# Kernel optimization log

Measured on AMD Instinct MI355X. Metric: run time of the kernel, lower is better.

Reference implementation:

```python
import jax, jax.numpy as jnp
import numpy as np

V, E, D = 100000, 128, 60  # vocab, embedding_size, d_alpha
B, J, M, P = 512, 101, 50, 5120
EPS = 1e-6


def setup_inputs() -> dict:
    key = jax.random.key(0)
    ks = jax.random.split(key, 12)
    s = 0.5 / E
    inp = {
        'batch_titems': jax.random.randint(ks[0], (B, J), 0, V),
        'batch_citems': jax.random.randint(ks[1], (B, M), 0, V),
        'batch_pad_ids': jax.random.randint(ks[2], (2, P), 0, M),
        't_emb': jax.random.uniform(ks[3], (V, E), jnp.float32, -s, s),
        'c_emb': jax.random.uniform(ks[4], (V, E), jnp.float32, -s, s),
        'Ac_w': jax.random.normal(ks[5], (D, E), jnp.float32) * 0.05,
        'Ac_b': jnp.zeros((D,), jnp.float32),
        'At_w': jax.random.normal(ks[6], (D, E), jnp.float32) * 0.05,
        'At_b': jnp.zeros((D,), jnp.float32),
        'Bc_w': jax.random.normal(ks[7], (E, E), jnp.float32) * 0.05,
        'Bc_b': jnp.zeros((E,), jnp.float32),
        'R_w': jax.random.normal(ks[8], (E, E), jnp.float32) * 0.05,
        'R_b': jnp.zeros((E,), jnp.float32),
    }
    return inp


def reference(batch_titems, batch_citems, batch_pad_ids, t_emb, c_emb,
              Ac_w, Ac_b, At_w, At_b, Bc_w, Bc_b, R_w, R_b):
    v = t_emb[batch_titems]            # [B, J, E] target item vectors
    u = c_emb[batch_citems]            # [B, M, E] context item vectors
    tp = v @ At_w.T + At_b             # [B, J, D]
    cp = u @ Ac_w.T + Ac_b             # [B, M, D]
    # cosine similarity with torch eps clamp on norms
    dot = jnp.einsum('bjd,bmd->bjm', tp, cp)
    nt = jnp.maximum(jnp.linalg.norm(tp, axis=-1), EPS)  # [B, J]
    nc = jnp.maximum(jnp.linalg.norm(cp, axis=-1), EPS)  # [B, M]
    cos = dot / (nt[:, :, None] * nc[:, None, :])        # [B, J, M]
    # pad mask: (batch, context-pos) pairs masked across all J target rows
    mask = jnp.zeros((cos.shape[0], cos.shape[2]), bool)
    mask = mask.at[batch_pad_ids[0], batch_pad_ids[1]].set(True)
    scores = jnp.where(mask[:, None, :], -jnp.inf, cos)
    attn = jax.nn.softmax(scores, axis=-1)               # [B, J, M]
    bu = u @ Bc_w.T + Bc_b                               # [B, M, E]
    alpha = jnp.einsum('bjm,bme->bje', attn, bu)         # [B, J, E]
    return alpha @ R_w.T + R_b                           # [B, J, E]
```

## Files before the change

### kernel.cpp

```cpp
#include <hip/hip_runtime.h>

typedef unsigned short u16;
typedef unsigned int   u32;
typedef short bf8 __attribute__((ext_vector_type(8)));
typedef float f4  __attribute__((ext_vector_type(4)));

#define NB   512
#define NJ   101
#define NM   50
#define NE   128
#define ND   60
#define NP   5120
#define NT   512
#define EPSV 1e-6f

#define U_B    0
#define T_B    17408
#define C_B    33536
#define H_B    42752
#define NT2_B  61184
#define NC2_B  61632
#define BAT_B  61888
#define BAC_B  62144
#define RB2_B  62400
#define MSK_B  62912
#define TIDX_B 63168
#define ARENA  63616

__device__ __forceinline__ u16 f2bh(float f) {
    return (u16)((__float_as_uint(f) + 0x8000u) >> 16);
}
__device__ __forceinline__ u32 pk2(float a, float b) {
    u32 ia = __float_as_uint(a) + 0x8000u;
    u32 ib = __float_as_uint(b) + 0x8000u;
    return (ia >> 16) | (ib & 0xFFFF0000u);
}
__device__ __forceinline__ bf8 gfrag(const float* p) {
    const float4* q = (const float4*)p;
    float4 x = q[0], y = q[1];
    union { u32 u[4]; bf8 v; } r;
    r.u[0] = pk2(x.x, x.y); r.u[1] = pk2(x.z, x.w);
    r.u[2] = pk2(y.x, y.y); r.u[3] = pk2(y.z, y.w);
    return r.v;
}

__global__ __launch_bounds__(128) void w2_kernel(
    const float* __restrict__ Bc_w, const float* __restrict__ Bc_b,
    const float* __restrict__ R_w,  const float* __restrict__ R_b,
    u16* __restrict__ w2t, float* __restrict__ rb2)
{
    const int e = blockIdx.x, k = threadIdx.x;
    const float* Rrow = R_w + e * NE;
    float acc = 0.f;
    #pragma unroll 8
    for (int j = 0; j < NE; j++) acc += Rrow[j] * Bc_w[j * NE + k];
    w2t[e * NE + k] = f2bh(acc);
    float c = Bc_b[k] * Rrow[k];
    for (int o = 32; o; o >>= 1) c += __shfl_xor(c, o, 64);
    __shared__ float part[2];
    if ((k & 63) == 0) part[k >> 6] = c;
    __syncthreads();
    if (k == 0) rb2[e] = part[0] + part[1] + R_b[e];
}

__global__ __launch_bounds__(NT, 4) void aitv_kernel(
    const int* __restrict__ titems, const int* __restrict__ citems,
    const int* __restrict__ pad_ids,
    const float* __restrict__ t_emb, const float* __restrict__ c_emb,
    const float* __restrict__ Ac_w,  const float* __restrict__ Ac_b,
    const float* __restrict__ At_w,  const float* __restrict__ At_b,
    const u16* __restrict__ w2t,     const float* __restrict__ rb2g,
    float* __restrict__ out)
{
    const int b    = blockIdx.x;
    const int t    = threadIdx.x;
    const int wid  = t >> 6;
    const int lane = t & 63;
    const int l15  = lane & 15;
    const int quad = lane >> 4;

    __shared__ __align__(16) char arena[ARENA];
    u16*   us16 = (u16*)(arena + U_B);   u32* us32 = (u32*)(arena + U_B);
    u16*   tp16 = (u16*)(arena + T_B);   u16* at16 = (u16*)(arena + T_B);
    u16*   cp16 = (u16*)(arena + C_B);
    u16*   hT16 = (u16*)(arena + H_B);
    float* nt2  = (float*)(arena + NT2_B);
    float* nc2  = (float*)(arena + NC2_B);
    float* bat  = (float*)(arena + BAT_B);
    float* bac  = (float*)(arena + BAC_B);
    float* rb2  = (float*)(arena + RB2_B);
    int*   msk  = (int*)(arena + MSK_B);
    int*   tidx = (int*)(arena + TIDX_B);

    for (int i = t; i < 64 * 64; i += NT) {
        int row = i >> 6, c2 = i & 63;
        u32 val = 0;
        if (row < NM) {
            int idx = citems[b * NM + row];
            float2 x = *(const float2*)(c_emb + (size_t)idx * NE + 2 * c2);
            val = pk2(x.x, x.y);
        }
        us32[row * 68 + c2] = val;
    }
    if (t < 112) { nt2[t] = 0.f; tidx[t] = titems[b * NJ + ((t < NJ) ? t : NJ - 1)]; }
    if (t >= 128 && t < 192) { int i = t - 128; nc2[i] = 0.f; msk[i] = 0; }
    if (t >= 192 && t < 256) {
        int i = t - 192;
        bat[i] = (i < ND) ? At_b[i] : 0.f;
        bac[i] = (i < ND) ? Ac_b[i] : 0.f;
    }
    if (t >= 256 && t < 384) rb2[t - 256] = rb2g[t - 256];
    __syncthreads();

    for (int i = t; i < NP; i += NT)
        if (pad_ids[i] == b) msk[pad_ids[NP + i]] = 1;

    for (int u = wid; u < 76; u += 8) {
        if (u < 28) {
            int jt = u >> 2, dt = u & 3;
            int d  = dt * 16 + l15;
            const float* vrow = t_emb + (size_t)tidx[jt * 16 + l15] * NE;
            const float* arow = At_w + (size_t)((d < ND) ? d : ND - 1) * NE;
            float bv = bat[d];
            f4 acc = {bv, bv, bv, bv};
            #pragma unroll
            for (int ks = 0; ks < 4; ks++) {
                bf8 a  = gfrag(vrow + ks * 32 + quad * 8);
                bf8 bb = gfrag(arow + ks * 32 + quad * 8);
                acc = __builtin_amdgcn_mfma_f32_16x16x32_bf16(a, bb, acc, 0, 0, 0);
            }
            int j0 = jt * 16 + quad * 4;
            #pragma unroll
            for (int r = 0; r < 4; r++) {
                float v = acc[r];
                tp16[(j0 + r) * 72 + d] = (d < ND) ? f2bh(v) : (u16)0;
                float q = (d < ND) ? v * v : 0.f;
                q += __shfl_xor(q, 1, 64); q += __shfl_xor(q, 2, 64);
                q += __shfl_xor(q, 4, 64); q += __shfl_xor(q, 8, 64);
                if (l15 == 0) atomicAdd(&nt2[j0 + r], q);
            }
        } else if (u < 44) {
            int uu = u - 28, mt = uu >> 2, dt = uu & 3;
            int d = dt * 16 + l15;
            const float* arow = Ac_w + (size_t)((d < ND) ? d : ND - 1) * NE;
            float bv = bac[d];
            f4 acc = {bv, bv, bv, bv};
            #pragma unroll
            for (int ks = 0; ks < 4; ks++) {
                bf8 a  = *(const bf8*)(us16 + (mt * 16 + l15) * 136 + ks * 32 + quad * 8);
                bf8 bb = gfrag(arow + ks * 32 + quad * 8);
                acc = __builtin_amdgcn_mfma_f32_16x16x32_bf16(a, bb, acc, 0, 0, 0);
            }
            int m0 = mt * 16 + quad * 4;
            #pragma unroll
            for (int r = 0; r < 4; r++) {
                float v = acc[r];
                cp16[(m0 + r) * 72 + d] = (d < ND) ? f2bh(v) : (u16)0;
                float q = (d < ND) ? v * v : 0.f;
                q += __shfl_xor(q, 1, 64); q += __shfl_xor(q, 2, 64);
                q += __shfl_xor(q, 4, 64); q += __shfl_xor(q, 8, 64);
                if (l15 == 0) atomicAdd(&nc2[m0 + r], q);
            }
        } else {
            int uu = u - 44, et = uu >> 2, mt = uu & 3;
            const u16* arow = w2t + (size_t)(et * 16 + l15) * NE;
            f4 acc = {0.f, 0.f, 0.f, 0.f};
            #pragma unroll
            for (int ks = 0; ks < 4; ks++) {
                bf8 a  = *(const bf8*)(arow + ks * 32 + quad * 8);
                bf8 bb = *(const bf8*)(us16 + (mt * 16 + l15) * 136 + ks * 32 + quad * 8);
                acc = __builtin_amdgcn_mfma_f32_16x16x32_bf16(a, bb, acc, 0, 0, 0);
            }
            int e0 = et * 16 + quad * 4;
            for (int r = 0; r < 4; r++)
                hT16[(e0 + r) * 72 + mt * 16 + l15] = f2bh(acc[r]);
        }
    }
    __syncthreads();

    if (wid < 7) {
        const int jt = wid;
        f4 S[4];
        #pragma unroll
        for (int mt = 0; mt < 4; mt++) {
            f4 acc = {0.f, 0.f, 0.f, 0.f};
            #pragma unroll
            for (int ks = 0; ks < 2; ks++) {
                bf8 a  = *(const bf8*)(tp16 + (jt * 16 + l15) * 72 + ks * 32 + quad * 8);
                bf8 bb = *(const bf8*)(cp16 + (mt * 16 + l15) * 72 + ks * 32 + quad * 8);
                acc = __builtin_amdgcn_mfma_f32_16x16x32_bf16(a, bb, acc, 0, 0, 0);
            }
            S[mt] = acc;
        }
        bool  valid[4]; float ncS[4];
        #pragma unroll
        for (int mt = 0; mt < 4; mt++) {
            int m = mt * 16 + l15;
            valid[mt] = (m < NM) && (msk[m] == 0);
            ncS[mt]   = valid[mt] ? fmaxf(sqrtf(nc2[m]), EPSV) : 1.f;
        }
        #pragma unroll
        for (int r = 0; r < 4; r++) {
            int j = jt * 16 + quad * 4 + r;
            float ntj = fmaxf(sqrtf(nt2[j]), EPSV);
            float x[4], mx = -INFINITY;
            #pragma unroll
            for (int mt = 0; mt < 4; mt++) {
                x[mt] = valid[mt] ? S[mt][r] / (ntj * ncS[mt]) : -INFINITY;
                mx = fmaxf(mx, x[mt]);
            }
            mx = fmaxf(mx, __shfl_xor(mx, 1, 64)); mx = fmaxf(mx, __shfl_xor(mx, 2, 64));
            mx = fmaxf(mx, __shfl_xor(mx, 4, 64)); mx = fmaxf(mx, __shfl_xor(mx, 8, 64));
            float p[4], sm = 0.f;
            #pragma unroll
            for (int mt = 0; mt < 4; mt++) {
                p[mt] = valid[mt] ? __expf(x[mt] - mx) : 0.f;
                sm += p[mt];
            }
            sm += __shfl_xor(sm, 1, 64); sm += __shfl_xor(sm, 2, 64);
            sm += __shfl_xor(sm, 4, 64); sm += __shfl_xor(sm, 8, 64);
            float inv = (sm > 0.f) ? 1.f / sm : 0.f;
            #pragma unroll
            for (int mt = 0; mt < 4; mt++)
                at16[j * 72 + mt * 16 + l15] = f2bh(p[mt] * inv);
        }
    }
    __syncthreads();

    for (int u = wid; u < 56; u += 8) {
        int jt = u >> 3, et = u & 7;
        float bv = rb2[et * 16 + l15];
        f4 acc = {bv, bv, bv, bv};
        #pragma unroll
        for (int ks = 0; ks < 2; ks++) {
            bf8 a  = *(const bf8*)(at16 + (jt * 16 + l15) * 72 + ks * 32 + quad * 8);
            bf8 bb = *(const bf8*)(hT16 + (et * 16 + l15) * 72 + ks * 32 + quad * 8);
            acc = __builtin_amdgcn_mfma_f32_16x16x32_bf16(a, bb, acc, 0, 0, 0);
        }
        int e = et * 16 + l15, j0 = jt * 16 + quad * 4;
        for (int r = 0; r < 4; r++) {
            int j = j0 + r;
            if (j < NJ) out[((size_t)b * NJ + j) * NE + e] = acc[r];
        }
    }
}

extern "C" void kernel_launch(void* const* d_in, const int* in_sizes, int n_in,
                              void* d_out, int out_size, void* d_ws, size_t ws_size,
                              hipStream_t stream) {
    const int*   titems  = (const int*)d_in[0];
    const int*   citems  = (const int*)d_in[1];
    const int*   pad_ids = (const int*)d_in[2];
    const float* t_emb   = (const float*)d_in[3];
    const float* c_emb   = (const float*)d_in[4];
    const float* Ac_w    = (const float*)d_in[5];
    const float* Ac_b    = (const float*)d_in[6];
    const float* At_w    = (const float*)d_in[7];
    const float* At_b    = (const float*)d_in[8];
    const float* Bc_w    = (const float*)d_in[9];
    const float* Bc_b    = (const float*)d_in[10];
    const float* R_w     = (const float*)d_in[11];
    const float* R_b     = (const float*)d_in[12];
    float* out = (float*)d_out;

    u16*   w2t = (u16*)d_ws;
    float* rb2 = (float*)((char*)d_ws + 32768);

    w2_kernel<<<NE, NE, 0, stream>>>(Bc_w, Bc_b, R_w, R_b, w2t, rb2);
    aitv_kernel<<<NB, NT, 0, stream>>>(titems, citems, pad_ids, t_emb, c_emb,
                                       Ac_w, Ac_b, At_w, At_b, w2t, rb2, out);
}
```

Before: 190.9 us.

## Keep gathered embedding fragments in registers and regroup per-wave projection work

The context embeddings are no longer staged into shared memory. Each wave now gathers a 16-row tile of target or context embeddings straight into register fragments and reuses them across all d-tiles, and for the context rows also across the Bc/R-fused e-tiles. This removes the LDS staging pass and the redundant re-gathering of t_emb rows that happened once per d-tile. Shared memory drops to about 44 KB, which could allow more blocks per CU. The trade-offs are that the work splits into 15 uneven groups across 8 waves, the context rows are gathered twice, and biases are read directly from global memory. The small w2 kernel also gets four independent accumulators.

```diff
diff --git a/kernel.cpp b/kernel.cpp
--- a/kernel.cpp
+++ b/kernel.cpp
@@ -14,18 +14,13 @@
 #define NT   512
 #define EPSV 1e-6f
 
-#define U_B    0
-#define T_B    17408
-#define C_B    33536
-#define H_B    42752
-#define NT2_B  61184
-#define NC2_B  61632
-#define BAT_B  61888
-#define BAC_B  62144
-#define RB2_B  62400
-#define MSK_B  62912
-#define TIDX_B 63168
-#define ARENA  63616
+#define T_B    0
+#define C_B    16128
+#define H_B    25344
+#define NT2_B  43776
+#define NC2_B  44224
+#define MSK_B  44480
+#define ARENA  44736
 
 __device__ __forceinline__ u16 f2bh(float f) {
     return (u16)((__float_as_uint(f) + 0x8000u) >> 16);
@@ -51,10 +46,15 @@
 {
     const int e = blockIdx.x, k = threadIdx.x;
     const float* Rrow = R_w + e * NE;
-    float acc = 0.f;
+    float a0 = 0.f, a1 = 0.f, a2 = 0.f, a3 = 0.f;
     #pragma unroll 8
-    for (int j = 0; j < NE; j++) acc += Rrow[j] * Bc_w[j * NE + k];
-    w2t[e * NE + k] = f2bh(acc);
+    for (int j = 0; j < NE; j += 4) {
+        a0 += Rrow[j]     * Bc_w[j * NE + k];
+        a1 += Rrow[j + 1] * Bc_w[(j + 1) * NE + k];
+        a2 += Rrow[j + 2] * Bc_w[(j + 2) * NE + k];
+        a3 += Rrow[j + 3] * Bc_w[(j + 3) * NE + k];
+    }
+    w2t[e * NE + k] = f2bh((a0 + a1) + (a2 + a3));
     float c = Bc_b[k] * Rrow[k];
     for (int o = 32; o; o >>= 1) c += __shfl_xor(c, o, 64);
     __shared__ float part[2];
@@ -80,100 +80,109 @@
     const int quad = lane >> 4;
 
     __shared__ __align__(16) char arena[ARENA];
-    u16*   us16 = (u16*)(arena + U_B);   u32* us32 = (u32*)(arena + U_B);
     u16*   tp16 = (u16*)(arena + T_B);   u16* at16 = (u16*)(arena + T_B);
     u16*   cp16 = (u16*)(arena + C_B);
     u16*   hT16 = (u16*)(arena + H_B);
     float* nt2  = (float*)(arena + NT2_B);
     float* nc2  = (float*)(arena + NC2_B);
-    float* bat  = (float*)(arena + BAT_B);
-    float* bac  = (float*)(arena + BAC_B);
-    float* rb2  = (float*)(arena + RB2_B);
     int*   msk  = (int*)(arena + MSK_B);
-    int*   tidx = (int*)(arena + TIDX_B);
-
-    for (int i = t; i < 64 * 64; i += NT) {
-        int row = i >> 6, c2 = i & 63;
-        u32 val = 0;
-        if (row < NM) {
-            int idx = citems[b * NM + row];
-            float2 x = *(const float2*)(c_emb + (size_t)idx * NE + 2 * c2);
-            val = pk2(x.x, x.y);
-        }
-        us32[row * 68 + c2] = val;
-    }
-    if (t < 112) { nt2[t] = 0.f; tidx[t] = titems[b * NJ + ((t < NJ) ? t : NJ - 1)]; }
-    if (t >= 128 && t < 192) { int i = t - 128; nc2[i] = 0.f; msk[i] = 0; }
-    if (t >= 192 && t < 256) {
-        int i = t - 192;
-        bat[i] = (i < ND) ? At_b[i] : 0.f;
-        bac[i] = (i < ND) ? Ac_b[i] : 0.f;
-    }
-    if (t >= 256 && t < 384) rb2[t - 256] = rb2g[t - 256];
+
+    if (t < 112) nt2[t] = 0.f;
+    else if (t < 176) nc2[t - 112] = 0.f;
+    else if (t < 240) msk[t - 176] = 0;
     __syncthreads();
 
     for (int i = t; i < NP; i += NT)
         if (pad_ids[i] == b) msk[pad_ids[NP + i]] = 1;
 
-    for (int u = wid; u < 76; u += 8) {
-        if (u < 28) {
-            int jt = u >> 2, dt = u & 3;
-            int d  = dt * 16 + l15;
-            const float* vrow = t_emb + (size_t)tidx[jt * 16 + l15] * NE;
-            const float* arow = At_w + (size_t)((d < ND) ? d : ND - 1) * NE;
-            float bv = bat[d];
-            f4 acc = {bv, bv, bv, bv};
-            #pragma unroll
-            for (int ks = 0; ks < 4; ks++) {
-                bf8 a  = gfrag(vrow + ks * 32 + quad * 8);
-                bf8 bb = gfrag(arow + ks * 32 + quad * 8);
-                acc = __builtin_amdgcn_mfma_f32_16x16x32_bf16(a, bb, acc, 0, 0, 0);
-            }
-            int j0 = jt * 16 + quad * 4;
-            #pragma unroll
-            for (int r = 0; r < 4; r++) {
-                float v = acc[r];
-                tp16[(j0 + r) * 72 + d] = (d < ND) ? f2bh(v) : (u16)0;
-                float q = (d < ND) ? v * v : 0.f;
-                q += __shfl_xor(q, 1, 64); q += __shfl_xor(q, 2, 64);
-                q += __shfl_xor(q, 4, 64); q += __shfl_xor(q, 8, 64);
-                if (l15 == 0) atomicAdd(&nt2[j0 + r], q);
-            }
-        } else if (u < 44) {
-            int uu = u - 28, mt = uu >> 2, dt = uu & 3;
-            int d = dt * 16 + l15;
-            const float* arow = Ac_w + (size_t)((d < ND) ? d : ND - 1) * NE;
-            float bv = bac[d];
-            f4 acc = {bv, bv, bv, bv};
-            #pragma unroll
-            for (int ks = 0; ks < 4; ks++) {
-                bf8 a  = *(const bf8*)(us16 + (mt * 16 + l15) * 136 + ks * 32 + quad * 8);
-                bf8 bb = gfrag(arow + ks * 32 + quad * 8);
-                acc = __builtin_amdgcn_mfma_f32_16x16x32_bf16(a, bb, acc, 0, 0, 0);
-            }
-            int m0 = mt * 16 + quad * 4;
-            #pragma unroll
-            for (int r = 0; r < 4; r++) {
-                float v = acc[r];
-                cp16[(m0 + r) * 72 + d] = (d < ND) ? f2bh(v) : (u16)0;
-                float q = (d < ND) ? v * v : 0.f;
-                q += __shfl_xor(q, 1, 64); q += __shfl_xor(q, 2, 64);
-                q += __shfl_xor(q, 4, 64); q += __shfl_xor(q, 8, 64);
-                if (l15 == 0) atomicAdd(&nc2[m0 + r], q);
+    for (int g = wid; g < 15; g += 8) {
+        if (g < 7) {
+            const int jt = g;
+            const int j  = jt * 16 + l15;
+            const float* vrow = t_emb + (size_t)titems[b * NJ + ((j < NJ) ? j : NJ - 1)] * NE;
+            bf8 A[4];
+            #pragma unroll
+            for (int ks = 0; ks < 4; ks++) A[ks] = gfrag(vrow + ks * 32 + quad * 8);
+            #pragma unroll
+            for (int dt = 0; dt < 4; dt++) {
+                const int d = dt * 16 + l15;
+                const float* arow = At_w + (size_t)((d < ND) ? d : 0) * NE;
+                float bv = (d < ND) ? At_b[d] : 0.f;
+                f4 acc = {bv, bv, bv, bv};
+                #pragma unroll
+                for (int ks = 0; ks < 4; ks++)
+                    acc = __builtin_amdgcn_mfma_f32_16x16x32_bf16(
+                        A[ks], gfrag(arow + ks * 32 + quad * 8), acc, 0, 0, 0);
+                const int j0 = jt * 16 + quad * 4;
+                #pragma unroll
+                for (int r = 0; r < 4; r++) {
+                    float v = acc[r];
+                    tp16[(j0 + r) * 72 + d] = (d < ND) ? f2bh(v) : (u16)0;
+                    float q = (d < ND) ? v * v : 0.f;
+                    q += __shfl_xor(q, 1, 64); q += __shfl_xor(q, 2, 64);
+                    q += __shfl_xor(q, 4, 64); q += __shfl_xor(q, 8, 64);
+                    if (l15 == 0) atomicAdd(&nt2[j0 + r], q);
+                }
+            }
+        } else if (g < 11) {
+            const int mt = g - 7;
+            const int m  = mt * 16 + l15;
+            const float* urow = c_emb + (size_t)citems[b * NM + ((m < NM) ? m : 0)] * NE;
+            bf8 U[4];
+            #pragma unroll
+            for (int ks = 0; ks < 4; ks++) U[ks] = gfrag(urow + ks * 32 + quad * 8);
+            #pragma unroll
+            for (int dt = 0; dt < 4; dt++) {
+                const int d = dt * 16 + l15;
+                const float* arow = Ac_w + (size_t)((d < ND) ? d : 0) * NE;
+                float bv = (d < ND) ? Ac_b[d] : 0.f;
+                f4 acc = {bv, bv, bv, bv};
+                #pragma unroll
+                for (int ks = 0; ks < 4; ks++)
+                    acc = __builtin_amdgcn_mfma_f32_16x16x32_bf16(
+                        U[ks], gfrag(arow + ks * 32 + quad * 8), acc, 0, 0, 0);
+                const int m0 = mt * 16 + quad * 4;
+                #pragma unroll
+                for (int r = 0; r < 4; r++) {
+                    float v = acc[r];
+                    cp16[(m0 + r) * 72 + d] = (d < ND) ? f2bh(v) : (u16)0;
+                    float q = (d < ND) ? v * v : 0.f;
+                    q += __shfl_xor(q, 1, 64); q += __shfl_xor(q, 2, 64);
+                    q += __shfl_xor(q, 4, 64); q += __shfl_xor(q, 8, 64);
+                    if (l15 == 0) atomicAdd(&nc2[m0 + r], q);
+                }
+            }
+            #pragma unroll
+            for (int et = 0; et < 4; et++) {
+                const u16* wrow = w2t + (size_t)(et * 16 + l15) * NE;
+                f4 acc = {0.f, 0.f, 0.f, 0.f};
+                #pragma unroll
+                for (int ks = 0; ks < 4; ks++)
+                    acc = __builtin_amdgcn_mfma_f32_16x16x32_bf16(
+                        *(const bf8*)(wrow + ks * 32 + quad * 8), U[ks], acc, 0, 0, 0);
+                const int e0 = et * 16 + quad * 4;
+                for (int r = 0; r < 4; r++)
+                    hT16[(e0 + r) * 72 + mt * 16 + l15] = f2bh(acc[r]);
             }
         } else {
-            int uu = u - 44, et = uu >> 2, mt = uu & 3;
-            const u16* arow = w2t + (size_t)(et * 16 + l15) * NE;
-            f4 acc = {0.f, 0.f, 0.f, 0.f};
-            #pragma unroll
-            for (int ks = 0; ks < 4; ks++) {
-                bf8 a  = *(const bf8*)(arow + ks * 32 + quad * 8);
-                bf8 bb = *(const bf8*)(us16 + (mt * 16 + l15) * 136 + ks * 32 + quad * 8);
-                acc = __builtin_amdgcn_mfma_f32_16x16x32_bf16(a, bb, acc, 0, 0, 0);
-            }
-            int e0 = et * 16 + quad * 4;
-            for (int r = 0; r < 4; r++)
-                hT16[(e0 + r) * 72 + mt * 16 + l15] = f2bh(acc[r]);
+            const int mt = g - 11;
+            const int m  = mt * 16 + l15;
+            const float* urow = c_emb + (size_t)citems[b * NM + ((m < NM) ? m : 0)] * NE;
+            bf8 U[4];
+            #pragma unroll
+            for (int ks = 0; ks < 4; ks++) U[ks] = gfrag(urow + ks * 32 + quad * 8);
+            #pragma unroll
+            for (int et = 4; et < 8; et++) {
+                const u16* wrow = w2t + (size_t)(et * 16 + l15) * NE;
+                f4 acc = {0.f, 0.f, 0.f, 0.f};
+                #pragma unroll
+                for (int ks = 0; ks < 4; ks++)
+                    acc = __builtin_amdgcn_mfma_f32_16x16x32_bf16(
+                        *(const bf8*)(wrow + ks * 32 + quad * 8), U[ks], acc, 0, 0, 0);
+                const int e0 = et * 16 + quad * 4;
+                for (int r = 0; r < 4; r++)
+                    hT16[(e0 + r) * 72 + mt * 16 + l15] = f2bh(acc[r]);
+            }
         }
     }
     __syncthreads();
@@ -192,7 +201,7 @@
             }
             S[mt] = acc;
         }
-        bool  valid[4]; float ncS[4];
+        bool valid[4]; float ncS[4];
         #pragma unroll
         for (int mt = 0; mt < 4; mt++) {
             int m = mt * 16 + l15;
@@ -229,7 +238,7 @@
 
     for (int u = wid; u < 56; u += 8) {
         int jt = u >> 3, et = u & 7;
-        float bv = rb2[et * 16 + l15];
+        float bv = rb2g[et * 16 + l15];
         f4 acc = {bv, bv, bv, bv};
         #pragma unroll
         for (int ks = 0; ks < 2; ks++) {
```

Measured after the change: 184.7 us. 3.2% less time.
